# Kernel optimization log

Hardware: AMD Instinct MI355X
Metric: run time of the kernel (lower is better)

Reference implementation:

```python
import jax, jax.numpy as jnp
import numpy as np

PATCH = 24  # self.current_patch
STRIDE = PATCH // 2


def _conv(x, w, b):
    # NCHW conv, SAME padding, stride 1 (= Conv2d(k=3, padding=1))
    y = jax.lax.conv_general_dilated(x, w, (1, 1), 'SAME',
                                     dimension_numbers=('NCHW', 'OIHW', 'NCHW'))
    return y + b[None, :, None, None]


def setup_inputs() -> dict:
    key = jax.random.key(0)
    ks = jax.random.split(key, 9)
    b, c, h, w = 2, 64, 192, 192
    s = 0.05  # keep sigmoid/tanh unsaturated
    return {
        'source': jax.random.normal(ks[0], (b, c, h, w), jnp.float32),
        'target': jax.random.normal(ks[1], (b, c, h, w), jnp.float32),
        # deform_net params (128->512->256->1)
        'W1': jax.random.normal(ks[2], (512, 128, 3, 3), jnp.float32) * s,
        'b1': jnp.zeros((512,), jnp.float32),
        'W2': jax.random.normal(ks[3], (256, 512, 3, 3), jnp.float32) * s,
        'b2': jnp.zeros((256,), jnp.float32),
        'W3': jax.random.normal(ks[4], (1, 256, 3, 3), jnp.float32) * s,
        'b3': jnp.zeros((1,), jnp.float32),
        # reg_net params (128->512->64->1); original declared 256 in-ch (bug), fixed to 128
        'Wr1': jax.random.normal(ks[5], (512, 128, 3, 3), jnp.float32) * s,
        'br1': jnp.zeros((512,), jnp.float32),
        'Wr2': jax.random.normal(ks[6], (64, 512, 3, 3), jnp.float32) * s,
        'br2': jnp.zeros((64,), jnp.float32),
        'Wr3': jax.random.normal(ks[7], (1, 64, 3, 3), jnp.float32) * s,
        'br3': jnp.zeros((1,), jnp.float32),
    }


def _attention(src, tgt, W1, b1, W2, b2, W3, b3):
    b, c, h, w = src.shape
    p, st = PATCH, STRIDE
    nH = (h - p) // st + 1
    nW = (w - p) // st + 1
    # patch gather indices
    r_idx = jnp.arange(nH)[:, None] * st + jnp.arange(p)[None, :]  # [nH, p]
    c_idx = jnp.arange(nW)[:, None] * st + jnp.arange(p)[None, :]  # [nW, p]
    # [b, c, nH, nW, p, p]
    def gather(x):
        return x[:, :, r_idx[:, None, :, None], c_idx[None, :, None, :]]
    ps = gather(src)
    pt = gather(tgt)
    # -> [b*nH*nW, 2c, p, p]  (one big batched conv replaces the python loop)
    pair = jnp.concatenate([ps, pt], axis=1)            # [b, 2c, nH, nW, p, p]
    pair = pair.transpose(0, 2, 3, 1, 4, 5).reshape(b * nH * nW, 2 * c, p, p)
    x = jax.nn.relu(_conv(pair, W1, b1))
    x = jax.nn.relu(_conv(x, W2, b2))
    score = jax.nn.sigmoid(_conv(x, W3, b3))            # [b*nH*nW, 1, p, p]
    score = score.reshape(b, nH, nW, 1, p, p).transpose(0, 3, 1, 2, 4, 5)  # [b,1,nH,nW,p,p]
    # overlap-add scatter (duplicate indices accumulate)
    R = jnp.broadcast_to(r_idx[:, None, :, None], (nH, nW, p, p))
    C = jnp.broadcast_to(c_idx[None, :, None, :], (nH, nW, p, p))
    att = jnp.zeros((b, 1, h, w), src.dtype).at[:, :, R, C].add(score)
    cnt = jnp.zeros((b, 1, h, w), src.dtype).at[:, :, R, C].add(1.0)
    return att / jnp.maximum(cnt, 1.0)


def reference(source, target, W1, b1, W2, b2, W3, b3, Wr1, br1, Wr2, br2, Wr3, br3):
    attention_map = _attention(source, target, W1, b1, W2, b2, W3, b3)
    x = jnp.concatenate([source, target], axis=1)       # [b, 128, h, w]
    x = jax.nn.relu(_conv(x, Wr1, br1))
    x = jax.nn.relu(_conv(x, Wr2, br2))
    registered = jnp.tanh(_conv(x, Wr3, br3))           # [b, 1, h, w]
    return registered, attention_map
```

## Files before the change

kernel.cpp:

```cpp
#include <hip/hip_runtime.h>
#include <cmath>

typedef _Float16 half8  __attribute__((ext_vector_type(8)));
typedef _Float16 half4v __attribute__((ext_vector_type(4)));
typedef float    float4v __attribute__((ext_vector_type(4)));

template<int MT, int NT, int MODE>
__global__ __launch_bounds__(256, 2)
void mfma_conv(const _Float16* __restrict__ in, const _Float16* __restrict__ Wg,
               const float* __restrict__ bias, _Float16* __restrict__ out,
               int CI, int CO, int RSin, int RSout, int NB, int NC, int p0)
{
    __shared__ __align__(16) _Float16 sW[9 * MT * 64 * 8];

    const int tid  = threadIdx.x;
    const int wave = tid >> 6;
    const int lane = tid & 63;
    const int ll   = lane & 15;
    const int quad = lane >> 4;

    const int NSUB = NC * (9 / NT);
    const int id   = blockIdx.x;
    const int xcd  = id & 7;
    const int slot = id >> 3;
    const int unit = (slot / NSUB) * 8 + xcd;
    const int rem  = slot % NSUB;
    const int pxb  = rem / NC;
    const int co_t = rem % NC;
    if (unit >= NB) return;
    const int co0 = co_t * (MT * 16);
    const int pbase = pxb * (NT * 64) + wave * (NT * 16);

    size_t in_base, out_base;
    int TY = 0, TX = 0;
    int b_off[NT], edge[NT];
    if (MODE == 0) {
        int pat = p0 + unit;
        int bb = pat / 225, remp = pat % 225;
        int pi = remp / 15, pj = remp % 15;
        in_base  = (size_t)bb * RSin * RSin * CI;
        out_base = (size_t)unit * 676 * CO;
        #pragma unroll
        for (int nt = 0; nt < NT; ++nt) {
            int p = pbase + nt * 16 + ll;
            int py = p / 24, px = p % 24;
            b_off[nt] = ((pi * 12 + py) * RSin + (pj * 12 + px)) * CI;
            edge[nt] = (py == 0 ? 1 : 0) | (py == 23 ? 2 : 0)
                     | (px == 0 ? 4 : 0) | (px == 23 ? 8 : 0);
        }
    } else if (MODE == 1) {
        in_base  = (size_t)unit * 676 * CI;
        out_base = (size_t)unit * 676 * CO;
        #pragma unroll
        for (int nt = 0; nt < NT; ++nt) {
            int p = pbase + nt * 16 + ll;
            b_off[nt] = ((p / 24) * RSin + (p % 24)) * CI;
            edge[nt] = 0;
        }
    } else {
        int tile = unit & 63, b = unit >> 6;
        TY = (tile >> 3) * 24; TX = (tile & 7) * 24;
        in_base  = (size_t)b * RSin * RSin * CI;
        out_base = (size_t)b * RSout * RSout * CO;
        #pragma unroll
        for (int nt = 0; nt < NT; ++nt) {
            int p = pbase + nt * 16 + ll;
            b_off[nt] = ((TY + p / 24) * RSin + (TX + p % 24)) * CI;
            edge[nt] = 0;
        }
    }

    float4v acc[MT][NT];
    #pragma unroll
    for (int mt = 0; mt < MT; ++mt)
        #pragma unroll
        for (int nt = 0; nt < NT; ++nt)
            acc[mt][nt] = (float4v){0.f, 0.f, 0.f, 0.f};

    for (int ci0 = 0; ci0 < CI; ci0 += 32) {
        __syncthreads();
        for (int c = tid; c < 9 * MT * 64; c += 256) {
            int lane_s = c & 63;
            int mtt = c >> 6;
            int mt = mtt % MT, t = mtt / MT;
            *(uint4*)&sW[(size_t)c * 8] =
                *(const uint4*)&Wg[((size_t)(co0 + mt * 16 + (lane_s & 15)) * 9 + t) * CI
                                   + ci0 + (lane_s >> 4) * 8];
        }
        __syncthreads();

        const _Float16* inp = in + in_base + ci0 + quad * 8;
        #pragma unroll
        for (int dy = 0; dy < 3; ++dy) {
            #pragma unroll
            for (int dx = 0; dx < 3; ++dx) {
                const int t = dy * 3 + dx;
                const int toff = (dy * RSin + dx) * CI;
                const int emask = (dy == 0 ? 1 : 0) | (dy == 2 ? 2 : 0)
                                | (dx == 0 ? 4 : 0) | (dx == 2 ? 8 : 0);
                half8 a[MT];
                #pragma unroll
                for (int mt = 0; mt < MT; ++mt)
                    a[mt] = *(const half8*)&sW[((t * MT + mt) * 64 + lane) * 8];
                #pragma unroll
                for (int nt = 0; nt < NT; ++nt) {
                    uint4 raw = *(const uint4*)(inp + b_off[nt] + toff);
                    if (MODE == 0) {
                        bool z = (edge[nt] & emask) != 0;
                        raw.x = z ? 0u : raw.x;
                        raw.y = z ? 0u : raw.y;
                        raw.z = z ? 0u : raw.z;
                        raw.w = z ? 0u : raw.w;
                    }
                    half8 b = *(half8*)&raw;
                    #pragma unroll
                    for (int mt = 0; mt < MT; ++mt)
                        acc[mt][nt] = __builtin_amdgcn_mfma_f32_16x16x32_f16(
                            a[mt], b, acc[mt][nt], 0, 0, 0);
                }
            }
        }
    }

    #pragma unroll
    for (int mt = 0; mt < MT; ++mt) {
        float4v bs = *(const float4v*)&bias[co0 + mt * 16 + quad * 4];
        #pragma unroll
        for (int nt = 0; nt < NT; ++nt) {
            int p = pbase + nt * 16 + ll;
            size_t ooff = out_base
                + (size_t)((TY + p / 24 + 1) * RSout + (TX + p % 24) + 1) * CO
                + co0 + mt * 16 + quad * 4;
            float4v v = acc[mt][nt];
            half4v h;
            h.x = (_Float16)fmaxf(v.x + bs.x, 0.f);
            h.y = (_Float16)fmaxf(v.y + bs.y, 0.f);
            h.z = (_Float16)fmaxf(v.z + bs.z, 0.f);
            h.w = (_Float16)fmaxf(v.w + bs.w, 0.f);
            *(half4v*)(out + ooff) = h;
        }
    }
}

static inline int swiz_grid(int NB, int NC, int PXB) {
    return ((NB + 7) & ~7) * NC * PXB;
}

template<int MODE, int ACT, int NT>
__global__ __launch_bounds__(256, 2)
void mfma_score(const _Float16* __restrict__ in, const _Float16* __restrict__ W16,
                const float* __restrict__ bias, float* __restrict__ outp,
                int CI, int RSI, int NB, int PXB)
{
    __shared__ __align__(16) _Float16 sW[9 * 16 * 32];

    const int tid  = threadIdx.x;
    const int wave = tid >> 6;
    const int lane = tid & 63;
    const int ll   = lane & 15;
    const int quad = lane >> 4;

    const int unit = blockIdx.x / PXB;
    const int pxb  = blockIdx.x % PXB;
    if (unit >= NB) return;
    const int pbase = pxb * (NT * 64) + wave * (NT * 16);

    size_t in_base;
    int ty = 0, tx = 0, bb = 0;
    if (MODE == 2) {
        bb = unit >> 6; int tile = unit & 63; ty = (tile >> 3) * 24; tx = (tile & 7) * 24;
        in_base = (size_t)bb * RSI * RSI * CI;
    } else {
        in_base = (size_t)unit * 676 * CI;
    }

    int b_off[NT];
    #pragma unroll
    for (int nt = 0; nt < NT; ++nt) {
        int p = pbase + nt * 16 + ll;
        b_off[nt] = ((ty + p / 24) * RSI + (tx + p % 24)) * CI;
    }

    float4v acc[NT];
    #pragma unroll
    for (int nt = 0; nt < NT; ++nt) acc[nt] = (float4v){0.f, 0.f, 0.f, 0.f};

    for (int ci0 = 0; ci0 < CI; ci0 += 32) {
        __syncthreads();
        for (int c = tid; c < 9 * 16 * 4; c += 256) {
            int q = c & 3, tco = c >> 2;
            int t = tco >> 4, co = tco & 15;
            *(uint4*)&sW[tco * 32 + q * 8] =
                *(const uint4*)&W16[((size_t)co * 9 + t) * CI + ci0 + q * 8];
        }
        __syncthreads();

        const _Float16* inp = in + in_base + ci0 + quad * 8;
        for (int dy = 0; dy < 3; ++dy)
            for (int dx = 0; dx < 3; ++dx) {
                const int t = dy * 3 + dx;
                const int toff = (dy * RSI + dx) * CI;
                half8 a = *(const half8*)&sW[(t * 16 + ll) * 32 + quad * 8];
                #pragma unroll
                for (int nt = 0; nt < NT; ++nt) {
                    half8 b = *(const half8*)(inp + b_off[nt] + toff);
                    acc[nt] = __builtin_amdgcn_mfma_f32_16x16x32_f16(a, b, acc[nt], 0, 0, 0);
                }
            }
    }

    if (quad == 0) {
        float bv = bias[0];
        #pragma unroll
        for (int nt = 0; nt < NT; ++nt) {
            int p = pbase + nt * 16 + ll;
            float v = acc[nt].x + bv;
            if (ACT == 1) {
                outp[(size_t)unit * 576 + p] = 1.f / (1.f + expf(-v));
            } else {
                int y = ty + p / 24, x = tx + p % 24;
                outp[(size_t)bb * 36864 + y * 192 + x] = tanhf(v);
            }
        }
    }
}

__global__ __launch_bounds__(256)
void build_x16i(const float* __restrict__ src, const float* __restrict__ tgt,
                _Float16* __restrict__ X)
{
    int idx = blockIdx.x * 256 + threadIdx.x;
    int q = idx & 15, pid = idx >> 4;
    if (pid >= 2 * 36864) return;
    int b = pid / 36864, r = pid % 36864;
    int y = r / 192, x = r % 192;
    half8 h;
    #pragma unroll
    for (int j = 0; j < 8; ++j) {
        int ch = q * 8 + j;
        const float* im = (ch < 64) ? src : tgt;
        h[j] = (_Float16)im[(size_t)(b * 64 + (ch & 63)) * 36864 + r];
    }
    *(half8*)&X[(((size_t)b * 194 + y + 1) * 194 + (x + 1)) * 128 + q * 8] = h;
}

__global__ __launch_bounds__(256)
void cvt_w(const float* __restrict__ src, _Float16* __restrict__ dst, int CO, int CI)
{
    int idx = blockIdx.x * 256 + threadIdx.x;
    if (idx >= CO * 9 * CI) return;
    int ci = idx % CI, t = (idx / CI) % 9, co = idx / (9 * CI);
    dst[idx] = (_Float16)src[((size_t)co * CI + ci) * 9 + t];
}

__global__ __launch_bounds__(256)
void cvt_pad16(const float* __restrict__ src, _Float16* __restrict__ dst, int CI)
{
    int idx = blockIdx.x * 256 + threadIdx.x;
    if (idx >= 16 * 9 * CI) return;
    int ci = idx % CI, t = (idx / CI) % 9, co = idx / (9 * CI);
    dst[idx] = (co == 0) ? (_Float16)src[(size_t)ci * 9 + t] : (_Float16)0.0f;
}

__global__ __launch_bounds__(256)
void ring_zero(_Float16* __restrict__ buf, int npatch, int RS, int CI)
{
    int c8 = CI >> 3;
    int RC = 2 * RS + 2 * (RS - 2);
    int idx = blockIdx.x * 256 + threadIdx.x;
    if (idx >= npatch * RC * c8) return;
    int q = idx % c8, rp = (idx / c8) % RC, pl = idx / (c8 * RC);
    int r, c;
    if (rp < RS)            { r = 0;      c = rp; }
    else if (rp < 2 * RS)   { r = RS - 1; c = rp - RS; }
    else {
        int s = rp - 2 * RS, half = RS - 2;
        if (s < half) { r = s + 1;        c = 0; }
        else          { r = s - half + 1; c = RS - 1; }
    }
    uint4 z = {0u, 0u, 0u, 0u};
    *(uint4*)&buf[((size_t)pl * RS * RS + r * RS + c) * CI + q * 8] = z;
}

__global__ __launch_bounds__(256)
void att_finalize(const float* __restrict__ score, float* __restrict__ out)
{
    int idx = blockIdx.x * 256 + threadIdx.x;
    if (idx >= 2 * 36864) return;
    int b = idx / 36864, r = idx % 36864;
    int y = r / 192, x = r % 192;
    int i_lo = (y >= 24) ? (y - 12) / 12 : 0;
    int i_hi = min(14, y / 12);
    int j_lo = (x >= 24) ? (x - 12) / 12 : 0;
    int j_hi = min(14, x / 12);
    float s = 0.f; int cnt = 0;
    for (int i = i_lo; i <= i_hi; ++i)
        for (int j = j_lo; j <= j_hi; ++j) {
            s += score[(((size_t)b * 15 + i) * 15 + j) * 576 + (y - 12 * i) * 24 + (x - 12 * j)];
            ++cnt;
        }
    out[idx] = s / (float)cnt;
}

extern "C" void kernel_launch(void* const* d_in, const int* in_sizes, int n_in,
                              void* d_out, int out_size, void* d_ws, size_t ws_size,
                              hipStream_t stream)
{
    const float* src = (const float*)d_in[0];
    const float* tgt = (const float*)d_in[1];
    const float* W1  = (const float*)d_in[2];  const float* b1  = (const float*)d_in[3];
    const float* W2  = (const float*)d_in[4];  const float* b2  = (const float*)d_in[5];
    const float* W3  = (const float*)d_in[6];  const float* b3  = (const float*)d_in[7];
    const float* Wr1 = (const float*)d_in[8];  const float* br1 = (const float*)d_in[9];
    const float* Wr2 = (const float*)d_in[10]; const float* br2 = (const float*)d_in[11];
    const float* Wr3 = (const float*)d_in[12]; const float* br3 = (const float*)d_in[13];
    float* out = (float*)d_out;

    _Float16* ws = (_Float16*)d_ws;
    size_t o = 0;
    _Float16* X16i = ws + o; o += (size_t)2 * 194 * 194 * 128;
    _Float16* W1h  = ws + o; o += (size_t)512 * 9 * 128;
    _Float16* W2h  = ws + o; o += (size_t)256 * 9 * 512;
    _Float16* Wr1h = ws + o; o += (size_t)512 * 9 * 128;
    _Float16* Wr2h = ws + o; o += (size_t)64 * 9 * 512;
    _Float16* W3p  = ws + o; o += (size_t)16 * 9 * 256;
    _Float16* Wr3p = ws + o; o += (size_t)16 * 9 * 64;
    float*    score = (float*)(ws + o); o += 2 * 259200;
    const size_t fixed_h = o;

    const size_t per_patch_h = (size_t)676 * (512 + 256);
    const size_t regA_h = (size_t)2 * 194 * 194 * 512;
    const size_t regB_h = (size_t)2 * 194 * 194 * 64;
    size_t h_avail = ws_size / 2;
    int P = 50;
    {
        size_t n450 = 450 * per_patch_h; if (n450 < regA_h + regB_h) n450 = regA_h + regB_h;
        size_t n150 = 150 * per_patch_h; if (n150 < regA_h + regB_h) n150 = regA_h + regB_h;
        if (h_avail >= fixed_h + n450)      P = 450;
        else if (h_avail >= fixed_h + n150) P = 150;
    }
    const int nchunks = 450 / P;

    _Float16* D1 = ws + fixed_h;
    _Float16* D2 = D1 + (size_t)P * 676 * 512;

    ring_zero<<<(2 * 772 * 16 + 255) / 256, 256, 0, stream>>>(X16i, 2, 194, 128);
    build_x16i<<<4608, 256, 0, stream>>>(src, tgt, X16i);
    cvt_w<<<2304, 256, 0, stream>>>(W1,  W1h,  512, 128);
    cvt_w<<<4608, 256, 0, stream>>>(W2,  W2h,  256, 512);
    cvt_w<<<2304, 256, 0, stream>>>(Wr1, Wr1h, 512, 128);
    cvt_w<<<1152, 256, 0, stream>>>(Wr2, Wr2h, 64,  512);
    cvt_pad16<<<(16 * 9 * 256 + 255) / 256, 256, 0, stream>>>(W3,  W3p,  256);
    cvt_pad16<<<(16 * 9 * 64  + 255) / 256, 256, 0, stream>>>(Wr3, Wr3p, 64);

    ring_zero<<<(P * 100 * 64 + 255) / 256, 256, 0, stream>>>(D1, P, 26, 512);
    ring_zero<<<(P * 100 * 32 + 255) / 256, 256, 0, stream>>>(D2, P, 26, 256);
    for (int c = 0; c < nchunks; ++c) {
        int p0 = c * P;
        mfma_conv<8, 3, 0><<<swiz_grid(P, 4, 3), 256, 0, stream>>>(
            X16i, W1h, b1, D1, 128, 512, 194, 26, P, 4, p0);
        mfma_conv<8, 3, 1><<<swiz_grid(P, 2, 3), 256, 0, stream>>>(
            D1, W2h, b2, D2, 512, 256, 26, 26, P, 2, 0);
        mfma_score<1, 1, 3><<<P * 3, 256, 0, stream>>>(
            D2, W3p, b3, score + (size_t)p0 * 576, 256, 26, P, 3);
    }
    att_finalize<<<288, 256, 0, stream>>>(score, out + 73728);

    {
        _Float16* A1 = ws + fixed_h;
        _Float16* A2 = A1 + ((P >= 150) ? regA_h : (size_t)194 * 194 * 512);
        if (P >= 150) {
            ring_zero<<<(2 * 772 * 64 + 255) / 256, 256, 0, stream>>>(A1, 2, 194, 512);
            ring_zero<<<(2 * 772 * 8  + 255) / 256, 256, 0, stream>>>(A2, 2, 194, 64);
            mfma_conv<8, 3, 2><<<swiz_grid(128, 4, 3), 256, 0, stream>>>(
                X16i, Wr1h, br1, A1, 128, 512, 194, 194, 128, 4, 0);
            mfma_conv<4, 3, 2><<<swiz_grid(128, 1, 3), 256, 0, stream>>>(
                A1, Wr2h, br2, A2, 512, 64, 194, 194, 128, 1, 0);
            mfma_score<2, 2, 3><<<128 * 3, 256, 0, stream>>>(
                A2, Wr3p, br3, out, 64, 194, 128, 3);
        } else {
            for (int b = 0; b < 2; ++b) {
                ring_zero<<<(772 * 64 + 255) / 256, 256, 0, stream>>>(A1, 1, 194, 512);
                ring_zero<<<(772 * 8  + 255) / 256, 256, 0, stream>>>(A2, 1, 194, 64);
                mfma_conv<8, 3, 2><<<swiz_grid(64, 4, 3), 256, 0, stream>>>(
                    X16i + (size_t)b * 194 * 194 * 128, Wr1h, br1, A1,
                    128, 512, 194, 194, 64, 4, 0);
                mfma_conv<4, 3, 2><<<swiz_grid(64, 1, 3), 256, 0, stream>>>(
                    A1, Wr2h, br2, A2, 512, 64, 194, 194, 64, 1, 0);
                mfma_score<2, 2, 3><<<64 * 3, 256, 0, stream>>>(
                    A2, Wr3p, br3, out + (size_t)b * 36864, 64, 194, 64, 3);
            }
        }
    }
}
```

Baseline: 2.308 ms.

## Split conv output-channel tile across two wave groups in 512-thread blocks

The conv kernel gains a COG parameter, so a block of 512 threads splits its 128-channel output tile between two groups of four waves, each holding accumulators for 64 channels (MT=4) instead of 128. The aim is to halve per-wave accumulator registers and raise occupancy, while the block still shares one weight tile in LDS and keeps the same grid. In exchange, each input pixel fragment is now loaded from global memory by two waves instead of one, and the larger blocks synchronise more threads per stage.

```diff
diff --git a/kernel.cpp b/kernel.cpp
--- a/kernel.cpp
+++ b/kernel.cpp
@@ -5,19 +5,21 @@
 typedef _Float16 half4v __attribute__((ext_vector_type(4)));
 typedef float    float4v __attribute__((ext_vector_type(4)));
 
-template<int MT, int NT, int MODE>
-__global__ __launch_bounds__(256, 2)
+template<int MT, int COG, int NT, int MODE>
+__global__ __launch_bounds__(256 * COG, COG == 2 ? 4 : 2)
 void mfma_conv(const _Float16* __restrict__ in, const _Float16* __restrict__ Wg,
                const float* __restrict__ bias, _Float16* __restrict__ out,
                int CI, int CO, int RSin, int RSout, int NB, int NC, int p0)
 {
-    __shared__ __align__(16) _Float16 sW[9 * MT * 64 * 8];
+    __shared__ __align__(16) _Float16 sW[9 * COG * MT * 64 * 8];
 
     const int tid  = threadIdx.x;
     const int wave = tid >> 6;
     const int lane = tid & 63;
     const int ll   = lane & 15;
     const int quad = lane >> 4;
+    const int px_g = wave & 3;
+    const int co_g = wave >> 2;
 
     const int NSUB = NC * (9 / NT);
     const int id   = blockIdx.x;
@@ -28,8 +30,8 @@
     const int pxb  = rem / NC;
     const int co_t = rem % NC;
     if (unit >= NB) return;
-    const int co0 = co_t * (MT * 16);
-    const int pbase = pxb * (NT * 64) + wave * (NT * 16);
+    const int co0 = co_t * (COG * MT * 16);
+    const int pbase = pxb * (NT * 64) + px_g * (NT * 16);
 
     size_t in_base, out_base;
     int TY = 0, TX = 0;
@@ -79,12 +81,12 @@
 
     for (int ci0 = 0; ci0 < CI; ci0 += 32) {
         __syncthreads();
-        for (int c = tid; c < 9 * MT * 64; c += 256) {
+        for (int c = tid; c < 9 * COG * MT * 64; c += 256 * COG) {
             int lane_s = c & 63;
             int mtt = c >> 6;
-            int mt = mtt % MT, t = mtt / MT;
+            int mtb = mtt % (COG * MT), t = mtt / (COG * MT);
             *(uint4*)&sW[(size_t)c * 8] =
-                *(const uint4*)&Wg[((size_t)(co0 + mt * 16 + (lane_s & 15)) * 9 + t) * CI
+                *(const uint4*)&Wg[((size_t)(co0 + mtb * 16 + (lane_s & 15)) * 9 + t) * CI
                                    + ci0 + (lane_s >> 4) * 8];
         }
         __syncthreads();
@@ -101,7 +103,8 @@
                 half8 a[MT];
                 #pragma unroll
                 for (int mt = 0; mt < MT; ++mt)
-                    a[mt] = *(const half8*)&sW[((t * MT + mt) * 64 + lane) * 8];
+                    a[mt] = *(const half8*)&sW[((t * (COG * MT) + co_g * MT + mt) * 64
+                                               + lane) * 8];
                 #pragma unroll
                 for (int nt = 0; nt < NT; ++nt) {
                     uint4 raw = *(const uint4*)(inp + b_off[nt] + toff);
@@ -124,13 +127,13 @@
 
     #pragma unroll
     for (int mt = 0; mt < MT; ++mt) {
-        float4v bs = *(const float4v*)&bias[co0 + mt * 16 + quad * 4];
+        float4v bs = *(const float4v*)&bias[co0 + (co_g * MT + mt) * 16 + quad * 4];
         #pragma unroll
         for (int nt = 0; nt < NT; ++nt) {
             int p = pbase + nt * 16 + ll;
             size_t ooff = out_base
                 + (size_t)((TY + p / 24 + 1) * RSout + (TX + p % 24) + 1) * CO
-                + co0 + mt * 16 + quad * 4;
+                + co0 + (co_g * MT + mt) * 16 + quad * 4;
             float4v v = acc[mt][nt];
             half4v h;
             h.x = (_Float16)fmaxf(v.x + bs.x, 0.f);
@@ -357,9 +360,9 @@
     ring_zero<<<(P * 100 * 32 + 255) / 256, 256, 0, stream>>>(D2, P, 26, 256);
     for (int c = 0; c < nchunks; ++c) {
         int p0 = c * P;
-        mfma_conv<8, 3, 0><<<swiz_grid(P, 4, 3), 256, 0, stream>>>(
+        mfma_conv<4, 2, 3, 0><<<swiz_grid(P, 4, 3), 512, 0, stream>>>(
             X16i, W1h, b1, D1, 128, 512, 194, 26, P, 4, p0);
-        mfma_conv<8, 3, 1><<<swiz_grid(P, 2, 3), 256, 0, stream>>>(
+        mfma_conv<4, 2, 3, 1><<<swiz_grid(P, 2, 3), 512, 0, stream>>>(
             D1, W2h, b2, D2, 512, 256, 26, 26, P, 2, 0);
         mfma_score<1, 1, 3><<<P * 3, 256, 0, stream>>>(
             D2, W3p, b3, score + (size_t)p0 * 576, 256, 26, P, 3);
@@ -372,9 +375,9 @@
         if (P >= 150) {
             ring_zero<<<(2 * 772 * 64 + 255) / 256, 256, 0, stream>>>(A1, 2, 194, 512);
             ring_zero<<<(2 * 772 * 8  + 255) / 256, 256, 0, stream>>>(A2, 2, 194, 64);
-            mfma_conv<8, 3, 2><<<swiz_grid(128, 4, 3), 256, 0, stream>>>(
+            mfma_conv<4, 2, 3, 2><<<swiz_grid(128, 4, 3), 512, 0, stream>>>(
                 X16i, Wr1h, br1, A1, 128, 512, 194, 194, 128, 4, 0);
-            mfma_conv<4, 3, 2><<<swiz_grid(128, 1, 3), 256, 0, stream>>>(
+            mfma_conv<4, 1, 3, 2><<<swiz_grid(128, 1, 3), 256, 0, stream>>>(
                 A1, Wr2h, br2, A2, 512, 64, 194, 194, 128, 1, 0);
             mfma_score<2, 2, 3><<<128 * 3, 256, 0, stream>>>(
                 A2, Wr3p, br3, out, 64, 194, 128, 3);
@@ -382,10 +385,10 @@
             for (int b = 0; b < 2; ++b) {
                 ring_zero<<<(772 * 64 + 255) / 256, 256, 0, stream>>>(A1, 1, 194, 512);
                 ring_zero<<<(772 * 8  + 255) / 256, 256, 0, stream>>>(A2, 1, 194, 64);
-                mfma_conv<8, 3, 2><<<swiz_grid(64, 4, 3), 256, 0, stream>>>(
+                mfma_conv<4, 2, 3, 2><<<swiz_grid(64, 4, 3), 512, 0, stream>>>(
                     X16i + (size_t)b * 194 * 194 * 128, Wr1h, br1, A1,
                     128, 512, 194, 194, 64, 4, 0);
-                mfma_conv<4, 3, 2><<<swiz_grid(64, 1, 3), 256, 0, stream>>>(
+                mfma_conv<4, 1, 3, 2><<<swiz_grid(64, 1, 3), 256, 0, stream>>>(
                     A1, Wr2h, br2, A2, 512, 64, 194, 194, 64, 1, 0);
                 mfma_score<2, 2, 3><<<64 * 3, 256, 0, stream>>>(
                     A2, Wr3p, br3, out + (size_t)b * 36864, 64, 194, 64, 3);
```

Measured after the change: 3.061 ms. +32.6%, slower.

## Double-buffer conv weights via direct global-to-LDS loads and retile blocks to 12 waves

Applied to the files above, without the earlier changes.

The MFMA conv kernel now stages weight tiles with async global_load_lds into a double-buffered LDS array, prefetching the next 32-channel slice while computing the current one, and needs one barrier per iteration instead of two. The output-channel tile is fixed at 4 MFMA tiles (64 channels), and blocks grow to 12 waves (6 for the reg_net second conv) covering all 576 patch pixels in one block, so weights are shared across more pixels per load. This trades fewer register-held accumulators per wave and larger blocks for better weight reuse and overlap of weight fetch with compute, but it changes occupancy and the grid shape.

```diff
diff --git a/kernel.cpp b/kernel.cpp
--- a/kernel.cpp
+++ b/kernel.cpp
@@ -5,13 +5,16 @@
 typedef _Float16 half4v __attribute__((ext_vector_type(4)));
 typedef float    float4v __attribute__((ext_vector_type(4)));
 
-template<int MT, int NT, int MODE>
-__global__ __launch_bounds__(256, 2)
+template<int WAVES, int NT, int MODE>
+__global__ __launch_bounds__(WAVES * 64, 3)
 void mfma_conv(const _Float16* __restrict__ in, const _Float16* __restrict__ Wg,
                const float* __restrict__ bias, _Float16* __restrict__ out,
-               int CI, int CO, int RSin, int RSout, int NB, int NC, int p0)
-{
-    __shared__ __align__(16) _Float16 sW[9 * MT * 64 * 8];
+               int CI, int CO, int RSin, int RSout, int NB, int NC, int PXB, int p0)
+{
+    constexpr int MT = 4;
+    constexpr int THREADS = WAVES * 64;
+    constexpr int CHUNKS = 9 * MT * 64;
+    __shared__ __align__(16) _Float16 sW[2][CHUNKS * 8];
 
     const int tid  = threadIdx.x;
     const int wave = tid >> 6;
@@ -19,7 +22,7 @@
     const int ll   = lane & 15;
     const int quad = lane >> 4;
 
-    const int NSUB = NC * (9 / NT);
+    const int NSUB = NC * PXB;
     const int id   = blockIdx.x;
     const int xcd  = id & 7;
     const int slot = id >> 3;
@@ -29,7 +32,7 @@
     const int co_t = rem % NC;
     if (unit >= NB) return;
     const int co0 = co_t * (MT * 16);
-    const int pbase = pxb * (NT * 64) + wave * (NT * 16);
+    const int pbase = (pxb * WAVES + wave) * (NT * 16);
 
     size_t in_base, out_base;
     int TY = 0, TX = 0;
@@ -70,6 +73,23 @@
         }
     }
 
+    auto stage = [&](int buf, int ci0) {
+        #pragma unroll
+        for (int k = 0; k < CHUNKS / THREADS; ++k) {
+            int c = tid + k * THREADS;
+            int lane_s = c & 63;
+            int mtt = c >> 6;
+            int mt = mtt & (MT - 1), t = mtt / MT;
+            const _Float16* src =
+                &Wg[((size_t)(co0 + mt * 16 + (lane_s & 15)) * 9 + t) * CI
+                    + ci0 + (lane_s >> 4) * 8];
+            __builtin_amdgcn_global_load_lds(
+                (const __attribute__((address_space(1))) void*)src,
+                (__attribute__((address_space(3))) void*)&sW[buf][(size_t)c * 8],
+                16, 0, 0);
+        }
+    };
+
     float4v acc[MT][NT];
     #pragma unroll
     for (int mt = 0; mt < MT; ++mt)
@@ -77,17 +97,12 @@
         for (int nt = 0; nt < NT; ++nt)
             acc[mt][nt] = (float4v){0.f, 0.f, 0.f, 0.f};
 
+    stage(0, 0);
+    __syncthreads();
+
+    int buf = 0;
     for (int ci0 = 0; ci0 < CI; ci0 += 32) {
-        __syncthreads();
-        for (int c = tid; c < 9 * MT * 64; c += 256) {
-            int lane_s = c & 63;
-            int mtt = c >> 6;
-            int mt = mtt % MT, t = mtt / MT;
-            *(uint4*)&sW[(size_t)c * 8] =
-                *(const uint4*)&Wg[((size_t)(co0 + mt * 16 + (lane_s & 15)) * 9 + t) * CI
-                                   + ci0 + (lane_s >> 4) * 8];
-        }
-        __syncthreads();
+        if (ci0 + 32 < CI) stage(buf ^ 1, ci0 + 32);
 
         const _Float16* inp = in + in_base + ci0 + quad * 8;
         #pragma unroll
@@ -101,7 +116,7 @@
                 half8 a[MT];
                 #pragma unroll
                 for (int mt = 0; mt < MT; ++mt)
-                    a[mt] = *(const half8*)&sW[((t * MT + mt) * 64 + lane) * 8];
+                    a[mt] = *(const half8*)&sW[buf][((t * MT + mt) * 64 + lane) * 8];
                 #pragma unroll
                 for (int nt = 0; nt < NT; ++nt) {
                     uint4 raw = *(const uint4*)(inp + b_off[nt] + toff);
@@ -120,6 +135,8 @@
                 }
             }
         }
+        __syncthreads();
+        buf ^= 1;
     }
 
     #pragma unroll
@@ -357,10 +374,10 @@
     ring_zero<<<(P * 100 * 32 + 255) / 256, 256, 0, stream>>>(D2, P, 26, 256);
     for (int c = 0; c < nchunks; ++c) {
         int p0 = c * P;
-        mfma_conv<8, 3, 0><<<swiz_grid(P, 4, 3), 256, 0, stream>>>(
-            X16i, W1h, b1, D1, 128, 512, 194, 26, P, 4, p0);
-        mfma_conv<8, 3, 1><<<swiz_grid(P, 2, 3), 256, 0, stream>>>(
-            D1, W2h, b2, D2, 512, 256, 26, 26, P, 2, 0);
+        mfma_conv<12, 3, 0><<<swiz_grid(P, 8, 1), 768, 0, stream>>>(
+            X16i, W1h, b1, D1, 128, 512, 194, 26, P, 8, 1, p0);
+        mfma_conv<12, 3, 1><<<swiz_grid(P, 4, 1), 768, 0, stream>>>(
+            D1, W2h, b2, D2, 512, 256, 26, 26, P, 4, 1, 0);
         mfma_score<1, 1, 3><<<P * 3, 256, 0, stream>>>(
             D2, W3p, b3, score + (size_t)p0 * 576, 256, 26, P, 3);
     }
@@ -372,21 +389,21 @@
         if (P >= 150) {
             ring_zero<<<(2 * 772 * 64 + 255) / 256, 256, 0, stream>>>(A1, 2, 194, 512);
             ring_zero<<<(2 * 772 * 8  + 255) / 256, 256, 0, stream>>>(A2, 2, 194, 64);
-            mfma_conv<8, 3, 2><<<swiz_grid(128, 4, 3), 256, 0, stream>>>(
-                X16i, Wr1h, br1, A1, 128, 512, 194, 194, 128, 4, 0);
-            mfma_conv<4, 3, 2><<<swiz_grid(128, 1, 3), 256, 0, stream>>>(
-                A1, Wr2h, br2, A2, 512, 64, 194, 194, 128, 1, 0);
+            mfma_conv<12, 3, 2><<<swiz_grid(128, 8, 1), 768, 0, stream>>>(
+                X16i, Wr1h, br1, A1, 128, 512, 194, 194, 128, 8, 1, 0);
+            mfma_conv<6, 3, 2><<<swiz_grid(128, 1, 2), 384, 0, stream>>>(
+                A1, Wr2h, br2, A2, 512, 64, 194, 194, 128, 1, 2, 0);
             mfma_score<2, 2, 3><<<128 * 3, 256, 0, stream>>>(
                 A2, Wr3p, br3, out, 64, 194, 128, 3);
         } else {
             for (int b = 0; b < 2; ++b) {
                 ring_zero<<<(772 * 64 + 255) / 256, 256, 0, stream>>>(A1, 1, 194, 512);
                 ring_zero<<<(772 * 8  + 255) / 256, 256, 0, stream>>>(A2, 1, 194, 64);
-                mfma_conv<8, 3, 2><<<swiz_grid(64, 4, 3), 256, 0, stream>>>(
+                mfma_conv<12, 3, 2><<<swiz_grid(64, 8, 1), 768, 0, stream>>>(
                     X16i + (size_t)b * 194 * 194 * 128, Wr1h, br1, A1,
-                    128, 512, 194, 194, 64, 4, 0);
-                mfma_conv<4, 3, 2><<<swiz_grid(64, 1, 3), 256, 0, stream>>>(
-                    A1, Wr2h, br2, A2, 512, 64, 194, 194, 64, 1, 0);
+                    128, 512, 194, 194, 64, 8, 1, 0);
+                mfma_conv<6, 3, 2><<<swiz_grid(64, 1, 2), 384, 0, stream>>>(
+                    A1, Wr2h, br2, A2, 512, 64, 194, 194, 64, 1, 2, 0);
                 mfma_score<2, 2, 3><<<64 * 3, 256, 0, stream>>>(
                     A2, Wr3p, br3, out + (size_t)b * 36864, 64, 194, 64, 3);
             }
```

Result: slower. 2.759 ms (+19.5%).

## Double-buffer weight tiles per kernel row using async global-to-LDS loads

Applied to the files above, without the earlier changes.

Weights for each 32-channel chunk are now staged one kernel row at a time into two LDS buffers using direct global-to-LDS loads, prefetching the next row while the current one feeds MFMAs. The earlier load-then-sync per channel chunk is replaced by explicit vmcnt waits and raw barriers, plus setprio around the compute. The aim is to hide weight-load latency and shrink the LDS footprint so occupancy can rise. The hand-tuned vmcnt counts assume a fixed number of outstanding loads, so any extra global loads in flight (the input reads) could make the waits wrong or overly conservative.

```diff
diff --git a/kernel.cpp b/kernel.cpp
--- a/kernel.cpp
+++ b/kernel.cpp
@@ -11,7 +11,9 @@
                const float* __restrict__ bias, _Float16* __restrict__ out,
                int CI, int CO, int RSin, int RSout, int NB, int NC, int p0)
 {
-    __shared__ __align__(16) _Float16 sW[9 * MT * 64 * 8];
+    constexpr int CHUNKS_PH = 3 * MT * 64;
+    constexpr int STAGE_N   = CHUNKS_PH / 256;
+    __shared__ __align__(16) _Float16 sW[2][CHUNKS_PH * 8];
 
     const int tid  = threadIdx.x;
     const int wave = tid >> 6;
@@ -70,6 +72,23 @@
         }
     }
 
+    auto stage = [&](int buf, int ci0, int dy) {
+        #pragma unroll
+        for (int k = 0; k < STAGE_N; ++k) {
+            int c = tid + k * 256;
+            int lane_s = c & 63;
+            int mtt = c >> 6;
+            int mt = mtt % MT, dxl = mtt / MT;
+            const _Float16* src =
+                &Wg[((size_t)(co0 + mt * 16 + (lane_s & 15)) * 9 + (dy * 3 + dxl)) * CI
+                    + ci0 + (lane_s >> 4) * 8];
+            __builtin_amdgcn_global_load_lds(
+                (const __attribute__((address_space(1))) void*)src,
+                (__attribute__((address_space(3))) void*)&sW[buf][(size_t)c * 8],
+                16, 0, 0);
+        }
+    };
+
     float4v acc[MT][NT];
     #pragma unroll
     for (int mt = 0; mt < MT; ++mt)
@@ -77,49 +96,56 @@
         for (int nt = 0; nt < NT; ++nt)
             acc[mt][nt] = (float4v){0.f, 0.f, 0.f, 0.f};
 
-    for (int ci0 = 0; ci0 < CI; ci0 += 32) {
-        __syncthreads();
-        for (int c = tid; c < 9 * MT * 64; c += 256) {
-            int lane_s = c & 63;
-            int mtt = c >> 6;
-            int mt = mtt % MT, t = mtt / MT;
-            *(uint4*)&sW[(size_t)c * 8] =
-                *(const uint4*)&Wg[((size_t)(co0 + mt * 16 + (lane_s & 15)) * 9 + t) * CI
-                                   + ci0 + (lane_s >> 4) * 8];
-        }
-        __syncthreads();
-
+    const int phases = (CI >> 5) * 3;
+    stage(0, 0, 0);
+
+    int buf = 0, ci0 = 0, dy = 0;
+    for (int ph = 0; ph < phases; ++ph) {
+        const int dy_n = (dy == 2) ? 0 : dy + 1;
+        const int ci_n = (dy == 2) ? ci0 + 32 : ci0;
+        if (ph + 1 < phases) {
+            stage(buf ^ 1, ci_n, dy_n);
+            if (MT == 8) asm volatile("s_waitcnt vmcnt(6)" ::: "memory");
+            else         asm volatile("s_waitcnt vmcnt(3)" ::: "memory");
+        } else {
+            asm volatile("s_waitcnt vmcnt(0)" ::: "memory");
+        }
+        __builtin_amdgcn_s_barrier();
+        __builtin_amdgcn_sched_barrier(0);
+
+        __builtin_amdgcn_s_setprio(1);
         const _Float16* inp = in + in_base + ci0 + quad * 8;
-        #pragma unroll
-        for (int dy = 0; dy < 3; ++dy) {
+        const int rowoff = dy * RSin * CI;
+        #pragma unroll
+        for (int dx = 0; dx < 3; ++dx) {
+            const int toff = rowoff + dx * CI;
+            const int emask = (dy == 0 ? 1 : 0) | (dy == 2 ? 2 : 0)
+                            | (dx == 0 ? 4 : 0) | (dx == 2 ? 8 : 0);
+            half8 a[MT];
             #pragma unroll
-            for (int dx = 0; dx < 3; ++dx) {
-                const int t = dy * 3 + dx;
-                const int toff = (dy * RSin + dx) * CI;
-                const int emask = (dy == 0 ? 1 : 0) | (dy == 2 ? 2 : 0)
-                                | (dx == 0 ? 4 : 0) | (dx == 2 ? 8 : 0);
-                half8 a[MT];
+            for (int mt = 0; mt < MT; ++mt)
+                a[mt] = *(const half8*)&sW[buf][((dx * MT + mt) * 64 + lane) * 8];
+            #pragma unroll
+            for (int nt = 0; nt < NT; ++nt) {
+                uint4 raw = *(const uint4*)(inp + b_off[nt] + toff);
+                if (MODE == 0) {
+                    bool z = (edge[nt] & emask) != 0;
+                    raw.x = z ? 0u : raw.x;
+                    raw.y = z ? 0u : raw.y;
+                    raw.z = z ? 0u : raw.z;
+                    raw.w = z ? 0u : raw.w;
+                }
+                half8 b = *(half8*)&raw;
                 #pragma unroll
                 for (int mt = 0; mt < MT; ++mt)
-                    a[mt] = *(const half8*)&sW[((t * MT + mt) * 64 + lane) * 8];
-                #pragma unroll
-                for (int nt = 0; nt < NT; ++nt) {
-                    uint4 raw = *(const uint4*)(inp + b_off[nt] + toff);
-                    if (MODE == 0) {
-                        bool z = (edge[nt] & emask) != 0;
-                        raw.x = z ? 0u : raw.x;
-                        raw.y = z ? 0u : raw.y;
-                        raw.z = z ? 0u : raw.z;
-                        raw.w = z ? 0u : raw.w;
-                    }
-                    half8 b = *(half8*)&raw;
-                    #pragma unroll
-                    for (int mt = 0; mt < MT; ++mt)
-                        acc[mt][nt] = __builtin_amdgcn_mfma_f32_16x16x32_f16(
-                            a[mt], b, acc[mt][nt], 0, 0, 0);
-                }
+                    acc[mt][nt] = __builtin_amdgcn_mfma_f32_16x16x32_f16(
+                        a[mt], b, acc[mt][nt], 0, 0, 0);
             }
         }
+        __builtin_amdgcn_s_setprio(0);
+        asm volatile("" ::: "memory");
+        __builtin_amdgcn_s_barrier();
+        buf ^= 1; dy = dy_n; ci0 = ci_n;
     }
 
     #pragma unroll
```

New measurement: 2.211 ms. -4.2%, faster.
